# Performance work log

Hardware: AMD Instinct MI355X
Metric: run time of the kernel (lower is better)

## Reference

```python
import jax, jax.numpy as jnp
import numpy as np

N = 2048  # number of graph nodes


def setup_inputs() -> dict:
    key = jax.random.key(0)
    k1, k2, k3, k4 = jax.random.split(key, 4)
    # dense non-negative adjacency / association matrix
    A = jax.random.uniform(k1, (N, N), dtype=jnp.float32)
    # GTConv weights: layer0.conv1, layer0.conv2, layer1.conv1 (each (2,1,1,1))
    w1a = jax.random.normal(k2, (2, 1, 1, 1), dtype=jnp.float32)
    w1b = jax.random.normal(k3, (2, 1, 1, 1), dtype=jnp.float32)
    w2a = jax.random.normal(k4, (2, 1, 1, 1), dtype=jnp.float32)
    return {"A": A, "w1a": w1a, "w1b": w1b, "w2a": w2a}


def _gtconv(A4, w):
    # A4: (1,1,n,n); w: (2,1,1,1). softmax over dim=1 (singleton -> ones),
    # broadcast-multiply -> (2,1,n,n), sum over dim 0 -> (1,n,n)
    sw = jax.nn.softmax(w, axis=1)
    return jnp.sum(A4 * sw, axis=0)


def _norm(H):
    # H: (n,n). H <- diag(deg)^-1 @ (H + I), expressed as a row-scale
    # (identical math to the diagonal mm in the original).
    n = H.shape[0]
    H = H + jnp.eye(n, dtype=H.dtype)
    deg = jnp.sum(H, axis=1)
    deg = jnp.where(deg <= 1e-10, jnp.ones_like(deg), deg)
    return H / deg[:, None]


def reference(A, w1a, w1b, w2a):
    A4 = A[None, None]  # (1,1,n,n) after the forward's unsqueeze + broadcast
    # layer 0 (first=True)
    a = _gtconv(A4, w1a)            # (1,n,n)
    b = _gtconv(A4, w1b)            # (1,n,n)
    H = jnp.matmul(a, b)            # (1,n,n)
    # layer 1 (first=False): normalization of H[0], then bmm with conv(A)
    H_ = _norm(H[0])[None]          # (1,n,n)
    a2 = _gtconv(A4, w2a)           # (1,n,n)
    H2 = jnp.matmul(H_, a2)         # (1,n,n)
    return H2
```

## Files before the change

kernel.cpp:

```cpp
#include <hip/hip_runtime.h>
#include <stdint.h>

#define N 2048
#define TILE 128
#define BK 64
#define KI (N / BK)
#define LDSW 72
#define NN ((size_t)N * (size_t)N)

typedef unsigned short u16;
typedef __bf16 bf16x8 __attribute__((ext_vector_type(8)));
typedef unsigned short ushortx8 __attribute__((ext_vector_type(8)));
typedef float floatx4 __attribute__((ext_vector_type(4)));

static __device__ __forceinline__ u16 f2bf(float f) {
  unsigned int u = __builtin_bit_cast(unsigned int, f);
  return (u16)((u + 0x7fffu + ((u >> 16) & 1u)) >> 16);
}
static __device__ __forceinline__ float bf2f(u16 h) {
  unsigned int u = ((unsigned int)h) << 16;
  return __builtin_bit_cast(float, u);
}

__global__ void cast_tr(const float* __restrict__ A, u16* __restrict__ Ab,
                        u16* __restrict__ Abt) {
  __shared__ float tile[32][33];
  const int tx = threadIdx.x, ty = threadIdx.y;
  const int c = blockIdx.x * 32 + tx;
#pragma unroll
  for (int i = 0; i < 4; i++) {
    const int r = blockIdx.y * 32 + ty + i * 8;
    const float v = A[(size_t)r * N + c];
    Ab[(size_t)r * N + c] = f2bf(v);
    tile[ty + i * 8][tx] = v;
  }
  __syncthreads();
  const int r2 = blockIdx.y * 32 + tx;
#pragma unroll
  for (int i = 0; i < 4; i++) {
    const int c2 = blockIdx.x * 32 + ty + i * 8;
    Abt[(size_t)c2 * N + r2] = f2bf(tile[tx][ty + i * 8]);
  }
}

__device__ __forceinline__ void gemm_core(const u16* __restrict__ L,
                                          const u16* __restrict__ Rt,
                                          floatx4 acc[4][2]) {
  __shared__ __align__(16) u16 As[2][TILE * LDSW];
  __shared__ __align__(16) u16 Bs[2][TILE * LDSW];

  const int t = threadIdx.x;
  const int row0 = blockIdx.y * TILE;
  const int col0 = blockIdx.x * TILE;

  const int srow = t >> 2;
  const int sc = (t & 3) * 16;
  const u16* gA = L + (size_t)(row0 + srow) * N + sc;
  const u16* gB = Rt + (size_t)(col0 + srow) * N + sc;
  const int woff = srow * LDSW + sc;

  const int lane = t & 63;
  const int w = t >> 6;
  const int wr = (w >> 2) * 64;
  const int wc = (w & 3) * 32;
  const int lr = lane & 15;
  const int q = lane >> 4;
  const int abase = (wr + lr) * LDSW + q * 8;
  const int bbase = (wc + lr) * LDSW + q * 8;

#pragma unroll
  for (int i = 0; i < 4; i++)
#pragma unroll
    for (int j = 0; j < 2; j++) acc[i][j] = (floatx4){0.f, 0.f, 0.f, 0.f};

  ushortx8 sA[2][2], sB[2][2];
  sA[0][0] = *(const ushortx8*)(gA);
  sA[0][1] = *(const ushortx8*)(gA + 8);
  sB[0][0] = *(const ushortx8*)(gB);
  sB[0][1] = *(const ushortx8*)(gB + 8);
  sA[1][0] = *(const ushortx8*)(gA + BK);
  sA[1][1] = *(const ushortx8*)(gA + BK + 8);
  sB[1][0] = *(const ushortx8*)(gB + BK);
  sB[1][1] = *(const ushortx8*)(gB + BK + 8);
  *(ushortx8*)&As[0][woff] = sA[0][0];
  *(ushortx8*)&As[0][woff + 8] = sA[0][1];
  *(ushortx8*)&Bs[0][woff] = sB[0][0];
  *(ushortx8*)&Bs[0][woff + 8] = sB[0][1];
  __syncthreads();

#define GSTEP(i, cur, nxt)                                                    \
  {                                                                           \
    if ((i) + 2 < KI) {                                                       \
      sA[cur][0] = *(const ushortx8*)(gA + ((i) + 2) * BK);                   \
      sA[cur][1] = *(const ushortx8*)(gA + ((i) + 2) * BK + 8);               \
      sB[cur][0] = *(const ushortx8*)(gB + ((i) + 2) * BK);                   \
      sB[cur][1] = *(const ushortx8*)(gB + ((i) + 2) * BK + 8);               \
    }                                                                         \
    _Pragma("unroll") for (int kk = 0; kk < 2; kk++) {                        \
      bf16x8 af[4], bfr[2];                                                   \
      _Pragma("unroll") for (int mt = 0; mt < 4; mt++) af[mt] =               \
          __builtin_bit_cast(bf16x8,                                          \
              *(const ushortx8*)&As[cur][abase + kk * 32 + mt * 16 * LDSW]);  \
      _Pragma("unroll") for (int nt = 0; nt < 2; nt++) bfr[nt] =              \
          __builtin_bit_cast(bf16x8,                                          \
              *(const ushortx8*)&Bs[cur][bbase + kk * 32 + nt * 16 * LDSW]);  \
      _Pragma("unroll") for (int mt = 0; mt < 4; mt++)                        \
          _Pragma("unroll") for (int nt = 0; nt < 2; nt++) acc[mt][nt] =      \
              __builtin_amdgcn_mfma_f32_16x16x32_bf16(af[mt], bfr[nt],        \
                                                      acc[mt][nt], 0, 0, 0);  \
    }                                                                         \
    if ((i) + 1 < KI) {                                                       \
      *(ushortx8*)&As[nxt][woff] = sA[nxt][0];                                \
      *(ushortx8*)&As[nxt][woff + 8] = sA[nxt][1];                            \
      *(ushortx8*)&Bs[nxt][woff] = sB[nxt][0];                                \
      *(ushortx8*)&Bs[nxt][woff + 8] = sB[nxt][1];                            \
    }                                                                         \
    __syncthreads();                                                          \
  }

  for (int io = 0; io < KI; io += 2) {
    GSTEP(io, 0, 1)
    GSTEP(io + 1, 1, 0)
  }
#undef GSTEP
}

__global__ __launch_bounds__(512, 2) void gemm_aa(const u16* __restrict__ Ab,
                                                  const u16* __restrict__ Abt,
                                                  u16* __restrict__ Mb) {
  floatx4 acc[4][2];
  gemm_core(Ab, Abt, acc);
  const int t = threadIdx.x;
  const int lane = t & 63, w = t >> 6;
  const int wr = (w >> 2) * 64, wc = (w & 3) * 32;
  const int lr = lane & 15, q = lane >> 4;
  const int row0 = blockIdx.y * TILE, col0 = blockIdx.x * TILE;
#pragma unroll
  for (int mt = 0; mt < 4; mt++)
#pragma unroll
    for (int r = 0; r < 4; r++) {
      const int rr = row0 + wr + mt * 16 + q * 4 + r;
#pragma unroll
      for (int nt = 0; nt < 2; nt++) {
        const int cc = col0 + wc + nt * 16 + lr;
        Mb[(size_t)rr * N + cc] = f2bf(acc[mt][nt][r]);
      }
    }
}

__global__ void rowsum_k(const u16* __restrict__ Mb, float* __restrict__ rdeg) {
  const int row = blockIdx.x;
  const int t = threadIdx.x;
  const ushortx8 v = *((const ushortx8*)(Mb + (size_t)row * N) + t);
  float s = 0.f;
#pragma unroll
  for (int j = 0; j < 8; j++) s += bf2f(v[j]);
#pragma unroll
  for (int off = 32; off > 0; off >>= 1) s += __shfl_down(s, off, 64);
  __shared__ float ws[4];
  if ((t & 63) == 0) ws[t >> 6] = s;
  __syncthreads();
  if (t == 0) {
    float d = 4.f * (ws[0] + ws[1] + ws[2] + ws[3]) + 1.f;
    if (d <= 1e-10f) d = 1.f;
    rdeg[row] = 1.f / d;
  }
}

__global__ __launch_bounds__(512, 2) void gemm_ma(const u16* __restrict__ Mb,
                                                  const u16* __restrict__ Abt,
                                                  const float* __restrict__ A,
                                                  const float* __restrict__ rdeg,
                                                  float* __restrict__ out) {
  floatx4 acc[4][2];
  gemm_core(Mb, Abt, acc);
  const int t = threadIdx.x;
  const int lane = t & 63, w = t >> 6;
  const int wr = (w >> 2) * 64, wc = (w & 3) * 32;
  const int lr = lane & 15, q = lane >> 4;
  const int row0 = blockIdx.y * TILE, col0 = blockIdx.x * TILE;
#pragma unroll
  for (int mt = 0; mt < 4; mt++)
#pragma unroll
    for (int r = 0; r < 4; r++) {
      const int rr = row0 + wr + mt * 16 + q * 4 + r;
      const float rd = rdeg[rr];
#pragma unroll
      for (int nt = 0; nt < 2; nt++) {
        const int cc = col0 + wc + nt * 16 + lr;
        out[(size_t)rr * N + cc] =
            (8.f * acc[mt][nt][r] + 2.f * A[(size_t)rr * N + cc]) * rd;
      }
    }
}

extern "C" void kernel_launch(void* const* d_in, const int* in_sizes, int n_in,
                              void* d_out, int out_size, void* d_ws, size_t ws_size,
                              hipStream_t stream) {
  const float* A = (const float*)d_in[0];
  float* out = (float*)d_out;
  char* ws = (char*)d_ws;
  u16* Ab = (u16*)ws;
  u16* Abt = (u16*)(ws + NN * 2);
  u16* Mb = (u16*)(ws + NN * 4);
  float* rdeg = (float*)(ws + NN * 6);

  cast_tr<<<dim3(N / 32, N / 32), dim3(32, 8), 0, stream>>>(A, Ab, Abt);
  gemm_aa<<<dim3(N / TILE, N / TILE), 512, 0, stream>>>(Ab, Abt, Mb);
  rowsum_k<<<N, 256, 0, stream>>>(Mb, rdeg);
  gemm_ma<<<dim3(N / TILE, N / TILE), 512, 0, stream>>>(Mb, Abt, A, rdeg, out);
}
```

Before: 134.9 us.

## Split GEMM K dimension across two warp groups with LDS reduction

Each GEMM block now runs 1024 threads split into two halves. Each half handles half of the K range with its own double-buffered LDS tiles, and the partial accumulators are combined through a shared-memory exchange where each half keeps one column subtile. The grid has only 256 blocks, so the intent is more in-flight waves per CU and better latency hiding. This doubles LDS usage and adds a reduction pass and an extra barrier, and the launch_bounds of 4 blocks of 1024 may cap registers per thread.

```diff
diff --git a/kernel.cpp b/kernel.cpp
--- a/kernel.cpp
+++ b/kernel.cpp
@@ -4,8 +4,9 @@
 #define N 2048
 #define TILE 128
 #define BK 64
-#define KI (N / BK)
+#define KH 16
 #define LDSW 72
+#define RSTR 17
 #define NN ((size_t)N * (size_t)N)
 
 typedef unsigned short u16;
@@ -46,23 +47,26 @@
 __device__ __forceinline__ void gemm_core(const u16* __restrict__ L,
                                           const u16* __restrict__ Rt,
                                           floatx4 acc[4][2]) {
-  __shared__ __align__(16) u16 As[2][TILE * LDSW];
-  __shared__ __align__(16) u16 Bs[2][TILE * LDSW];
-
-  const int t = threadIdx.x;
+  __shared__ __align__(16) u16 As[2][2][TILE * LDSW];
+  __shared__ __align__(16) u16 Bs[2][2][TILE * LDSW];
+
+  const int t = threadIdx.x;
+  const int h = t >> 9;
+  const int tl = t & 511;
   const int row0 = blockIdx.y * TILE;
   const int col0 = blockIdx.x * TILE;
 
-  const int srow = t >> 2;
-  const int sc = (t & 3) * 16;
-  const u16* gA = L + (size_t)(row0 + srow) * N + sc;
-  const u16* gB = Rt + (size_t)(col0 + srow) * N + sc;
+  const int srow = tl >> 2;
+  const int sc = (tl & 3) * 16;
+  const u16* gA = L + (size_t)(row0 + srow) * N + h * (KH * BK) + sc;
+  const u16* gB = Rt + (size_t)(col0 + srow) * N + h * (KH * BK) + sc;
   const int woff = srow * LDSW + sc;
 
   const int lane = t & 63;
   const int w = t >> 6;
-  const int wr = (w >> 2) * 64;
-  const int wc = (w & 3) * 32;
+  const int sub = w & 7;
+  const int wr = (sub >> 2) * 64;
+  const int wc = (sub & 3) * 32;
   const int lr = lane & 15;
   const int q = lane >> 4;
   const int abase = (wr + lr) * LDSW + q * 8;
@@ -82,15 +86,15 @@
   sA[1][1] = *(const ushortx8*)(gA + BK + 8);
   sB[1][0] = *(const ushortx8*)(gB + BK);
   sB[1][1] = *(const ushortx8*)(gB + BK + 8);
-  *(ushortx8*)&As[0][woff] = sA[0][0];
-  *(ushortx8*)&As[0][woff + 8] = sA[0][1];
-  *(ushortx8*)&Bs[0][woff] = sB[0][0];
-  *(ushortx8*)&Bs[0][woff + 8] = sB[0][1];
+  *(ushortx8*)&As[h][0][woff] = sA[0][0];
+  *(ushortx8*)&As[h][0][woff + 8] = sA[0][1];
+  *(ushortx8*)&Bs[h][0][woff] = sB[0][0];
+  *(ushortx8*)&Bs[h][0][woff + 8] = sB[0][1];
   __syncthreads();
 
 #define GSTEP(i, cur, nxt)                                                    \
   {                                                                           \
-    if ((i) + 2 < KI) {                                                       \
+    if ((i) + 2 < KH) {                                                       \
       sA[cur][0] = *(const ushortx8*)(gA + ((i) + 2) * BK);                   \
       sA[cur][1] = *(const ushortx8*)(gA + ((i) + 2) * BK + 8);               \
       sB[cur][0] = *(const ushortx8*)(gB + ((i) + 2) * BK);                   \
@@ -100,51 +104,65 @@
       bf16x8 af[4], bfr[2];                                                   \
       _Pragma("unroll") for (int mt = 0; mt < 4; mt++) af[mt] =               \
           __builtin_bit_cast(bf16x8,                                          \
-              *(const ushortx8*)&As[cur][abase + kk * 32 + mt * 16 * LDSW]);  \
+              *(const ushortx8*)&As[h][cur][abase + kk * 32 + mt * 16 * LDSW]); \
       _Pragma("unroll") for (int nt = 0; nt < 2; nt++) bfr[nt] =              \
           __builtin_bit_cast(bf16x8,                                          \
-              *(const ushortx8*)&Bs[cur][bbase + kk * 32 + nt * 16 * LDSW]);  \
+              *(const ushortx8*)&Bs[h][cur][bbase + kk * 32 + nt * 16 * LDSW]); \
       _Pragma("unroll") for (int mt = 0; mt < 4; mt++)                        \
           _Pragma("unroll") for (int nt = 0; nt < 2; nt++) acc[mt][nt] =      \
               __builtin_amdgcn_mfma_f32_16x16x32_bf16(af[mt], bfr[nt],        \
                                                       acc[mt][nt], 0, 0, 0);  \
     }                                                                         \
-    if ((i) + 1 < KI) {                                                       \
-      *(ushortx8*)&As[nxt][woff] = sA[nxt][0];                                \
-      *(ushortx8*)&As[nxt][woff + 8] = sA[nxt][1];                            \
-      *(ushortx8*)&Bs[nxt][woff] = sB[nxt][0];                                \
-      *(ushortx8*)&Bs[nxt][woff + 8] = sB[nxt][1];                            \
+    if ((i) + 1 < KH) {                                                       \
+      *(ushortx8*)&As[h][nxt][woff] = sA[nxt][0];                             \
+      *(ushortx8*)&As[h][nxt][woff + 8] = sA[nxt][1];                         \
+      *(ushortx8*)&Bs[h][nxt][woff] = sB[nxt][0];                             \
+      *(ushortx8*)&Bs[h][nxt][woff + 8] = sB[nxt][1];                         \
     }                                                                         \
     __syncthreads();                                                          \
   }
 
-  for (int io = 0; io < KI; io += 2) {
+  for (int io = 0; io < KH; io += 2) {
     GSTEP(io, 0, 1)
     GSTEP(io + 1, 1, 0)
   }
 #undef GSTEP
-}
-
-__global__ __launch_bounds__(512, 2) void gemm_aa(const u16* __restrict__ Ab,
-                                                  const u16* __restrict__ Abt,
-                                                  u16* __restrict__ Mb) {
+
+  float* red = (float*)&As[0][0][0];
+  const int oh = 1 - h;
+  const int rship = (sub * 2 + oh) * (64 * RSTR);
+  const int rkeep = (sub * 2 + h) * (64 * RSTR);
+#pragma unroll
+  for (int mt = 0; mt < 4; mt++)
+#pragma unroll
+    for (int r = 0; r < 4; r++)
+      red[rship + (mt * 16 + q * 4 + r) * RSTR + lr] = acc[mt][oh][r];
+  __syncthreads();
+#pragma unroll
+  for (int mt = 0; mt < 4; mt++)
+#pragma unroll
+    for (int r = 0; r < 4; r++)
+      acc[mt][h][r] += red[rkeep + (mt * 16 + q * 4 + r) * RSTR + lr];
+}
+
+__global__ __launch_bounds__(1024, 4) void gemm_aa(const u16* __restrict__ Ab,
+                                                   const u16* __restrict__ Abt,
+                                                   u16* __restrict__ Mb) {
   floatx4 acc[4][2];
   gemm_core(Ab, Abt, acc);
   const int t = threadIdx.x;
   const int lane = t & 63, w = t >> 6;
-  const int wr = (w >> 2) * 64, wc = (w & 3) * 32;
+  const int sub = w & 7, h = w >> 3;
+  const int wr = (sub >> 2) * 64, wc = (sub & 3) * 32;
   const int lr = lane & 15, q = lane >> 4;
   const int row0 = blockIdx.y * TILE, col0 = blockIdx.x * TILE;
+  const int cc = col0 + wc + h * 16 + lr;
 #pragma unroll
   for (int mt = 0; mt < 4; mt++)
 #pragma unroll
     for (int r = 0; r < 4; r++) {
       const int rr = row0 + wr + mt * 16 + q * 4 + r;
-#pragma unroll
-      for (int nt = 0; nt < 2; nt++) {
-        const int cc = col0 + wc + nt * 16 + lr;
-        Mb[(size_t)rr * N + cc] = f2bf(acc[mt][nt][r]);
-      }
+      Mb[(size_t)rr * N + cc] = f2bf(acc[mt][h][r]);
     }
 }
 
@@ -167,30 +185,27 @@
   }
 }
 
-__global__ __launch_bounds__(512, 2) void gemm_ma(const u16* __restrict__ Mb,
-                                                  const u16* __restrict__ Abt,
-                                                  const float* __restrict__ A,
-                                                  const float* __restrict__ rdeg,
-                                                  float* __restrict__ out) {
+__global__ __launch_bounds__(1024, 4) void gemm_ma(const u16* __restrict__ Mb,
+                                                   const u16* __restrict__ Abt,
+                                                   const float* __restrict__ A,
+                                                   const float* __restrict__ rdeg,
+                                                   float* __restrict__ out) {
   floatx4 acc[4][2];
   gemm_core(Mb, Abt, acc);
   const int t = threadIdx.x;
   const int lane = t & 63, w = t >> 6;
-  const int wr = (w >> 2) * 64, wc = (w & 3) * 32;
+  const int sub = w & 7, h = w >> 3;
+  const int wr = (sub >> 2) * 64, wc = (sub & 3) * 32;
   const int lr = lane & 15, q = lane >> 4;
   const int row0 = blockIdx.y * TILE, col0 = blockIdx.x * TILE;
+  const int cc = col0 + wc + h * 16 + lr;
 #pragma unroll
   for (int mt = 0; mt < 4; mt++)
 #pragma unroll
     for (int r = 0; r < 4; r++) {
       const int rr = row0 + wr + mt * 16 + q * 4 + r;
-      const float rd = rdeg[rr];
-#pragma unroll
-      for (int nt = 0; nt < 2; nt++) {
-        const int cc = col0 + wc + nt * 16 + lr;
-        out[(size_t)rr * N + cc] =
-            (8.f * acc[mt][nt][r] + 2.f * A[(size_t)rr * N + cc]) * rd;
-      }
+      out[(size_t)rr * N + cc] =
+          (8.f * acc[mt][h][r] + 2.f * A[(size_t)rr * N + cc]) * rdeg[rr];
     }
 }
 
@@ -206,7 +221,7 @@
   float* rdeg = (float*)(ws + NN * 6);
 
   cast_tr<<<dim3(N / 32, N / 32), dim3(32, 8), 0, stream>>>(A, Ab, Abt);
-  gemm_aa<<<dim3(N / TILE, N / TILE), 512, 0, stream>>>(Ab, Abt, Mb);
+  gemm_aa<<<dim3(N / TILE, N / TILE), 1024, 0, stream>>>(Ab, Abt, Mb);
   rowsum_k<<<N, 256, 0, stream>>>(Mb, rdeg);
-  gemm_ma<<<dim3(N / TILE, N / TILE), 512, 0, stream>>>(Mb, Abt, A, rdeg, out);
-}
+  gemm_ma<<<dim3(N / TILE, N / TILE), 1024, 0, stream>>>(Mb, Abt, A, rdeg, out);
+}
```

New measurement: 186.2 us. 1.38x slower.
